# Performance work log

Hardware: AMD Instinct MI355X
Metric: run time of the kernel (lower is better)

## Reference

```python
import jax, jax.numpy as jnp
import numpy as np

N_HEADS = 16
HEAD_SZ = 64

def setup_inputs() -> dict:
    key = jax.random.key(0)
    ks = jax.random.split(key, 6)
    E = 1024
    s = 1.0 / np.sqrt(E)
    return {
        "x": jax.random.normal(ks[0], (2, 2048, E), dtype=jnp.float32),
        "Wq": jax.random.normal(ks[1], (E, N_HEADS * HEAD_SZ), dtype=jnp.float32) * s,
        "Wk": jax.random.normal(ks[2], (E, N_HEADS * HEAD_SZ), dtype=jnp.float32) * s,
        "Wv": jax.random.normal(ks[3], (E, N_HEADS * HEAD_SZ), dtype=jnp.float32) * s,
        "Wp": jax.random.normal(ks[4], (N_HEADS * HEAD_SZ, E), dtype=jnp.float32) * s,
        "bp": jnp.zeros((E,), dtype=jnp.float32),
    }

def reference(x, Wq, Wk, Wv, Wp, bp):
    # flavor="masked": causal self-attention, pdrop=0 -> dropout is identity
    B, S, E = x.shape
    H, D = N_HEADS, HEAD_SZ
    q = (x @ Wq).reshape(B, S, H, D).transpose(0, 2, 1, 3)  # [B,H,S,D]
    k = (x @ Wk).reshape(B, S, H, D).transpose(0, 2, 1, 3)
    v = (x @ Wv).reshape(B, S, H, D).transpose(0, 2, 1, 3)
    scores = jnp.einsum("bhqd,bhkd->bhqk", q, k) / jnp.sqrt(jnp.float32(D))
    causal = jnp.tril(jnp.ones((S, S), dtype=bool))  # [S,S]
    scores = jnp.where(causal, scores, -jnp.inf)
    attn = jax.nn.softmax(scores, axis=-1)
    out = jnp.einsum("bhqk,bhkd->bhqd", attn, v)  # [B,H,S,D]
    out = out.transpose(0, 2, 1, 3).reshape(B, S, H * D)
    return out @ Wp + bp
```

## Files before the change

### kernel.cpp

```cpp
#include <hip/hip_runtime.h>
#include <hip/hip_bf16.h>
#include <math.h>

using bf16 = __hip_bfloat16;
typedef __attribute__((ext_vector_type(8))) short short8;
typedef __attribute__((ext_vector_type(4))) float floatx4;

#define MFMA16(a, b, c) __builtin_amdgcn_mfma_f32_16x16x32_bf16((a), (b), (c), 0, 0, 0)

__device__ __forceinline__ void gll16(const void* g, void* l) {
  __builtin_amdgcn_global_load_lds((__attribute__((address_space(1))) void*)(uintptr_t)g,
                                   (__attribute__((address_space(3))) void*)l, 16, 0, 0);
}

__global__ void detect_bias_k(const unsigned short* __restrict__ x,
                              const void* __restrict__ bsrc,
                              bf16* __restrict__ bdst, int* __restrict__ flag) {
  __shared__ int cnt;
  if (threadIdx.x == 0) cnt = 0;
  __syncthreads();
  int local = 0;
  for (int i = threadIdx.x; i < 8192; i += 256) {
    unsigned short v = x[2 * i];
    if (((v >> 7) & 0xFF) == 0xFF) local++;
  }
  if (local) atomicAdd(&cnt, local);
  __syncthreads();
  int f = (cnt > 0) ? 1 : 0;
  if (threadIdx.x == 0) *flag = f;
  for (int i = threadIdx.x; i < 1024; i += 256)
    bdst[i] = f ? __float2bfloat16(((const float*)bsrc)[i]) : ((const bf16*)bsrc)[i];
}

__global__ __launch_bounds__(256) void prep_k(const void* __restrict__ xin,
                                              bf16* __restrict__ xb,
                                              const void* __restrict__ W0,
                                              const void* __restrict__ W1,
                                              const void* __restrict__ W2,
                                              const void* __restrict__ W3,
                                              bf16* __restrict__ Wt,
                                              bf16* __restrict__ Wpt,
                                              const int* __restrict__ flag) {
  bool f32 = (*flag != 0);
  int z = blockIdx.z;
  if (z < 2) {
    int tid = threadIdx.y * 32 + threadIdx.x;
    int blockLin = z * 1024 + blockIdx.y * 32 + blockIdx.x;
    int idx = blockLin * 2048 + tid * 8;
    if (f32) {
      const float4* p = reinterpret_cast<const float4*>((const float*)xin + idx);
      float4 a = p[0], b = p[1];
      union { bf16 h[8]; uint4 u; } U;
      U.h[0] = __float2bfloat16(a.x); U.h[1] = __float2bfloat16(a.y);
      U.h[2] = __float2bfloat16(a.z); U.h[3] = __float2bfloat16(a.w);
      U.h[4] = __float2bfloat16(b.x); U.h[5] = __float2bfloat16(b.y);
      U.h[6] = __float2bfloat16(b.z); U.h[7] = __float2bfloat16(b.w);
      *reinterpret_cast<uint4*>(xb + idx) = U.u;
    } else {
      *reinterpret_cast<uint4*>(xb + idx) =
          *reinterpret_cast<const uint4*>((const bf16*)xin + idx);
    }
    return;
  }
  const void* src = (z == 2) ? W0 : (z == 3) ? W1 : (z == 4) ? W2 : W3;
  bf16* dst = (z == 5) ? Wpt : (Wt + (size_t)(z - 2) * 1024 * 1024);
  __shared__ float tsh[32][33];
  int tx = threadIdx.x, ty = threadIdx.y;
  int k0 = blockIdx.y * 32, n0 = blockIdx.x * 32;
  for (int i = 0; i < 4; i++) {
    size_t off = (size_t)(k0 + ty + i * 8) * 1024 + n0 + tx;
    tsh[ty + i * 8][tx] = f32 ? ((const float*)src)[off]
                              : __bfloat162float(((const bf16*)src)[off]);
  }
  __syncthreads();
  for (int i = 0; i < 4; i++)
    dst[(size_t)(n0 + ty + i * 8) * 1024 + k0 + tx] = __float2bfloat16(tsh[tx][ty + i * 8]);
}

__global__ __launch_bounds__(512) void vtrans_k(const bf16* __restrict__ QKV,
                                                bf16* __restrict__ VT) {
  __shared__ bf16 t[64][66];
  int tx = threadIdx.x, ty = threadIdx.y;
  int s0 = blockIdx.x * 64, bh = blockIdx.y;
  int b = bh >> 4, h = bh & 15;
  size_t rowb = (size_t)b * 2048;
  int hv = 2048 + h * 64;
#pragma unroll
  for (int i = 0; i < 8; i++)
    t[i * 8 + ty][tx] = QKV[(rowb + s0 + i * 8 + ty) * 3072 + hv + tx];
  __syncthreads();
#pragma unroll
  for (int i = 0; i < 8; i++)
    VT[((size_t)bh * 64 + i * 8 + ty) * 2048 + s0 + tx] = t[tx][i * 8 + ty];
}

__global__ __launch_bounds__(256) void gemm_bt128(const bf16* __restrict__ A, int lda,
                                                  const bf16* __restrict__ Bt, int ldb,
                                                  void* __restrict__ C, int ldc,
                                                  const bf16* __restrict__ bias, int K,
                                                  const int* __restrict__ outflag) {
  __shared__ bf16 As[2][128 * 32];
  __shared__ bf16 Bs[2][128 * 32];
  int t = threadIdx.x;
  int w = t >> 6, lane = t & 63;
  int g = lane >> 4, c = lane & 15;
  int wm = (w >> 1) * 64, wn = (w & 1) * 64;
  int m0 = blockIdx.y * 128, n0 = blockIdx.x * 128;

  int sr = w * 32 + (lane >> 2);
  int sc = (lane & 3) * 8;
  const bf16* Ab = A + (size_t)(m0 + sr) * lda + sc;
  const bf16* Bb = Bt + (size_t)(n0 + sr) * ldb + sc;
  int lofs = (w * 32) * 32;

  floatx4 acc[4][4] = {};

  for (int k0 = 0; k0 < K; k0 += 64) {
    __syncthreads();
#pragma unroll
    for (int h = 0; h < 2; h++) {
      gll16(Ab + k0 + h * 32, &As[h][lofs]);
      gll16(Ab + k0 + h * 32 + (size_t)16 * lda, &As[h][lofs + 16 * 32]);
      gll16(Bb + k0 + h * 32, &Bs[h][lofs]);
      gll16(Bb + k0 + h * 32 + (size_t)16 * ldb, &Bs[h][lofs + 16 * 32]);
    }
    __syncthreads();
#pragma unroll
    for (int h = 0; h < 2; h++) {
      short8 af[4], bf[4];
#pragma unroll
      for (int i = 0; i < 4; i++) {
        af[i] = *reinterpret_cast<const short8*>(&As[h][(wm + i * 16 + c) * 32 + g * 8]);
        bf[i] = *reinterpret_cast<const short8*>(&Bs[h][(wn + i * 16 + c) * 32 + g * 8]);
      }
#pragma unroll
      for (int i = 0; i < 4; i++)
#pragma unroll
        for (int j = 0; j < 4; j++) acc[i][j] = MFMA16(af[i], bf[j], acc[i][j]);
    }
  }

  bool f32out = (outflag != nullptr) && (*outflag != 0);
#pragma unroll
  for (int i = 0; i < 4; i++) {
    int rbase = m0 + wm + i * 16 + g * 4;
#pragma unroll
    for (int j = 0; j < 4; j++) {
      int col = n0 + wn + j * 16 + c;
      float bv = bias ? __bfloat162float(bias[col]) : 0.f;
#pragma unroll
      for (int r = 0; r < 4; r++) {
        size_t off = (size_t)(rbase + r) * ldc + col;
        float v = acc[i][j][r] + bv;
        if (f32out) ((float*)C)[off] = v;
        else ((bf16*)C)[off] = __float2bfloat16(v);
      }
    }
  }
}

__global__ __launch_bounds__(256) void gemm_bt64(const bf16* __restrict__ A, int lda,
                                                 const bf16* __restrict__ Bt, int ldb,
                                                 void* __restrict__ C, int ldc,
                                                 const bf16* __restrict__ bias, int K,
                                                 const int* __restrict__ outflag) {
  __shared__ bf16 As[2][128 * 32];
  __shared__ bf16 Bs[2][64 * 32];
  int t = threadIdx.x;
  int w = t >> 6, lane = t & 63;
  int g = lane >> 4, c = lane & 15;
  int wm = (w >> 1) * 64, wn = (w & 1) * 32;
  int m0 = blockIdx.y * 128, n0 = blockIdx.x * 64;

  int sr = (lane >> 2);
  int sc = (lane & 3) * 8;
  const bf16* Ab = A + (size_t)(m0 + w * 32 + sr) * lda + sc;
  const bf16* Bb = Bt + (size_t)(n0 + w * 16 + sr) * ldb + sc;
  int laofs = (w * 32) * 32;
  int lbofs = (w * 16) * 32;

  floatx4 acc[4][2] = {};

  for (int k0 = 0; k0 < K; k0 += 64) {
    __syncthreads();
#pragma unroll
    for (int h = 0; h < 2; h++) {
      gll16(Ab + k0 + h * 32, &As[h][laofs]);
      gll16(Ab + k0 + h * 32 + (size_t)16 * lda, &As[h][laofs + 16 * 32]);
      gll16(Bb + k0 + h * 32, &Bs[h][lbofs]);
    }
    __syncthreads();
#pragma unroll
    for (int h = 0; h < 2; h++) {
      short8 af[4], bf[2];
#pragma unroll
      for (int i = 0; i < 4; i++)
        af[i] = *reinterpret_cast<const short8*>(&As[h][(wm + i * 16 + c) * 32 + g * 8]);
#pragma unroll
      for (int j = 0; j < 2; j++)
        bf[j] = *reinterpret_cast<const short8*>(&Bs[h][(wn + j * 16 + c) * 32 + g * 8]);
#pragma unroll
      for (int i = 0; i < 4; i++)
#pragma unroll
        for (int j = 0; j < 2; j++) acc[i][j] = MFMA16(af[i], bf[j], acc[i][j]);
    }
  }

  bool f32out = (outflag != nullptr) && (*outflag != 0);
#pragma unroll
  for (int i = 0; i < 4; i++) {
    int rbase = m0 + wm + i * 16 + g * 4;
#pragma unroll
    for (int j = 0; j < 2; j++) {
      int col = n0 + wn + j * 16 + c;
      float bv = bias ? __bfloat162float(bias[col]) : 0.f;
#pragma unroll
      for (int r = 0; r < 4; r++) {
        size_t off = (size_t)(rbase + r) * ldc + col;
        float v = acc[i][j][r] + bv;
        if (f32out) ((float*)C)[off] = v;
        else ((bf16*)C)[off] = __float2bfloat16(v);
      }
    }
  }
}

__global__ __launch_bounds__(512, 4) void attn_lds2(bf16* __restrict__ QKV,
                                                    const bf16* __restrict__ VT) {
  const int S = 2048, LD = 3072;
  __shared__ bf16 Ks[2][2][64 * 32];
  __shared__ bf16 Vs[2][2][64 * 32];
  __shared__ bf16 Pb[8][16 * 72];

  int t = threadIdx.x, w = t >> 6, lane = t & 63, g = lane >> 4, c = lane & 15;
  int bx = blockIdx.x, bh = blockIdx.y;
  int qt = (bh >= 16) ? bx : (15 - bx);
  int b = bh >> 4, h = bh & 15;
  int qbase = qt * 128;
  size_t rowb = (size_t)b * S;
  int hq = h * 64, hk = 1024 + h * 64;
  const bf16* Vt = VT + (size_t)bh * 64 * 2048;
  bf16* pb = Pb[w];

  int su = (w & 3) * 16 + (lane >> 2);
  int sc = (lane & 3) * 8;
  const bf16* Kg = &QKV[(rowb + su) * LD + hk + sc];
  const bf16* Vg = &Vt[(size_t)su * 2048 + sc];
  int sofs = ((w & 3) * 16) * 32;

  short8 qf[2];
#pragma unroll
  for (int hf = 0; hf < 2; hf++)
    qf[hf] = *reinterpret_cast<const short8*>(
        &QKV[(rowb + qbase + w * 16 + c) * LD + hq + hf * 32 + g * 8]);

  floatx4 o[4] = {};
  float l_r[4] = {};

  int nkt = 2 * qt + 2;
  if (w < 4) {
    gll16(Kg, &Ks[0][0][sofs]);
    gll16(Kg + 32, &Ks[0][1][sofs]);
  } else {
    gll16(Vg, &Vs[0][0][sofs]);
    gll16(Vg + 32, &Vs[0][1][sofs]);
  }

  for (int kt = 0; kt < nkt; kt++) {
    int kbase = kt * 64;
    int cur = kt & 1;
    __syncthreads();
    if (kt + 1 < nkt) {
      int nb = cur ^ 1;
      size_t kofs = (size_t)(kbase + 64);
      if (w < 4) {
        gll16(Kg + kofs * LD, &Ks[nb][0][sofs]);
        gll16(Kg + kofs * LD + 32, &Ks[nb][1][sofs]);
      } else {
        gll16(Vg + kofs, &Vs[nb][0][sofs]);
        gll16(Vg + kofs + 32, &Vs[nb][1][sofs]);
      }
    }

    short8 kf[4][2];
#pragma unroll
    for (int nt = 0; nt < 4; nt++)
#pragma unroll
      for (int hf = 0; hf < 2; hf++)
        kf[nt][hf] =
            *reinterpret_cast<const short8*>(&Ks[cur][hf][(nt * 16 + c) * 32 + g * 8]);

    floatx4 s[4];
#pragma unroll
    for (int nt = 0; nt < 4; nt++) {
      floatx4 z = {};
      z = MFMA16(qf[0], kf[nt][0], z);
      z = MFMA16(qf[1], kf[nt][1], z);
      s[nt] = z;
    }

    int qrow = qbase + w * 16 + g * 4;
    bool diag = (kbase + 63 > qbase + w * 16);
#pragma unroll
    for (int nt = 0; nt < 4; nt++) {
      int kcol = kbase + nt * 16 + c;
#pragma unroll
      for (int r = 0; r < 4; r++) {
        float arg = fmaf(s[nt][r], 0.18033688f, -23.083120f);
        if (diag && (kcol > qrow + r)) arg = -1e30f;
        float p = exp2f(arg);
        l_r[r] += p;
        s[nt][r] = p;
      }
    }

    asm volatile("s_waitcnt lgkmcnt(0)" ::: "memory");
#pragma unroll
    for (int nt = 0; nt < 4; nt++)
#pragma unroll
      for (int r = 0; r < 4; r++)
        pb[(g * 4 + r) * 72 + nt * 16 + c] = __float2bfloat16(s[nt][r]);
    asm volatile("s_waitcnt lgkmcnt(0)" ::: "memory");
    short8 pf0 = *reinterpret_cast<const short8*>(&pb[c * 72 + g * 8]);
    short8 pf1 = *reinterpret_cast<const short8*>(&pb[c * 72 + 32 + g * 8]);

#pragma unroll
    for (int dt = 0; dt < 4; dt++) {
      short8 vf0 = *reinterpret_cast<const short8*>(&Vs[cur][0][(dt * 16 + c) * 32 + g * 8]);
      short8 vf1 = *reinterpret_cast<const short8*>(&Vs[cur][1][(dt * 16 + c) * 32 + g * 8]);
      o[dt] = MFMA16(pf0, vf0, o[dt]);
      o[dt] = MFMA16(pf1, vf1, o[dt]);
    }
  }

#pragma unroll
  for (int r = 0; r < 4; r++) {
    float v = l_r[r];
    v += __shfl_xor(v, 1); v += __shfl_xor(v, 2);
    v += __shfl_xor(v, 4); v += __shfl_xor(v, 8);
    l_r[r] = 1.0f / v;
  }

#pragma unroll
  for (int dt = 0; dt < 4; dt++)
#pragma unroll
    for (int r = 0; r < 4; r++) {
      float v = o[dt][r] * l_r[r];
      QKV[(rowb + qbase + w * 16 + g * 4 + r) * LD + hq + dt * 16 + c] =
          __float2bfloat16(v);
    }
}

extern "C" void kernel_launch(void* const* d_in, const int* in_sizes, int n_in,
                              void* d_out, int out_size, void* d_ws, size_t ws_size,
                              hipStream_t stream) {
  char* ws = (char*)d_ws;
  const size_t MB = 1024 * 1024;
  int* flag = (int*)ws;
  bf16* bias = (bf16*)(ws + 4096);
  bf16* xb = (bf16*)(ws + 1 * MB);
  bf16* Wt = (bf16*)(ws + 9 * MB);
  bf16* Wpt = (bf16*)(ws + 15 * MB);
  bf16* QKV = (bf16*)(ws + 17 * MB);
  bf16* VT = xb;

  detect_bias_k<<<1, 256, 0, stream>>>((const unsigned short*)d_in[0], d_in[5], bias, flag);
  prep_k<<<dim3(32, 32, 6), dim3(32, 8), 0, stream>>>(d_in[0], xb, d_in[1], d_in[2],
                                                      d_in[3], d_in[4], Wt, Wpt, flag);

  gemm_bt128<<<dim3(24, 32), 256, 0, stream>>>(xb, 1024, Wt, 1024, QKV, 3072, nullptr,
                                               1024, nullptr);
  vtrans_k<<<dim3(32, 32), dim3(64, 8), 0, stream>>>(QKV, VT);
  attn_lds2<<<dim3(16, 32), 512, 0, stream>>>(QKV, VT);
  gemm_bt64<<<dim3(16, 32), 256, 0, stream>>>(QKV, 3072, Wpt, 1024, d_out, 1024, bias,
                                              1024, flag);
}
```

Baseline: 203.0 us.

## Fuse V transpose into QKV GEMM epilogue and XOR-swizzle LDS tiles

The QKV projection GEMM now writes Q and K into a 2048-wide buffer and writes V directly in transposed per-head layout from its epilogue. This removes the separate vtrans kernel launch and its extra pass over V. In addition, the LDS tiles in all GEMM and attention kernels use an XOR swizzle on the 16-byte column chunk, which is meant to cut LDS bank conflicts on the short8 fragment reads. The transposed V store writes 8-byte chunks with stride 2048 elements, so those global writes are poorly coalesced.

```diff
diff --git a/kernel.cpp b/kernel.cpp
--- a/kernel.cpp
+++ b/kernel.cpp
@@ -77,28 +77,10 @@
     dst[(size_t)(n0 + ty + i * 8) * 1024 + k0 + tx] = __float2bfloat16(tsh[tx][ty + i * 8]);
 }
 
-__global__ __launch_bounds__(512) void vtrans_k(const bf16* __restrict__ QKV,
-                                                bf16* __restrict__ VT) {
-  __shared__ bf16 t[64][66];
-  int tx = threadIdx.x, ty = threadIdx.y;
-  int s0 = blockIdx.x * 64, bh = blockIdx.y;
-  int b = bh >> 4, h = bh & 15;
-  size_t rowb = (size_t)b * 2048;
-  int hv = 2048 + h * 64;
-#pragma unroll
-  for (int i = 0; i < 8; i++)
-    t[i * 8 + ty][tx] = QKV[(rowb + s0 + i * 8 + ty) * 3072 + hv + tx];
-  __syncthreads();
-#pragma unroll
-  for (int i = 0; i < 8; i++)
-    VT[((size_t)bh * 64 + i * 8 + ty) * 2048 + s0 + tx] = t[tx][i * 8 + ty];
-}
-
-__global__ __launch_bounds__(256) void gemm_bt128(const bf16* __restrict__ A, int lda,
-                                                  const bf16* __restrict__ Bt, int ldb,
-                                                  void* __restrict__ C, int ldc,
-                                                  const bf16* __restrict__ bias, int K,
-                                                  const int* __restrict__ outflag) {
+__global__ __launch_bounds__(256) void gemm_qkv(const bf16* __restrict__ A, int lda,
+                                                const bf16* __restrict__ Bt, int ldb,
+                                                bf16* __restrict__ QKV2,
+                                                bf16* __restrict__ VT, int K) {
   __shared__ bf16 As[2][128 * 32];
   __shared__ bf16 Bs[2][128 * 32];
   int t = threadIdx.x;
@@ -108,10 +90,11 @@
   int m0 = blockIdx.y * 128, n0 = blockIdx.x * 128;
 
   int sr = w * 32 + (lane >> 2);
-  int sc = (lane & 3) * 8;
-  const bf16* Ab = A + (size_t)(m0 + sr) * lda + sc;
-  const bf16* Bb = Bt + (size_t)(n0 + sr) * ldb + sc;
+  int scz = (((lane & 3) ^ ((lane >> 3) & 3)) * 8);
+  const bf16* Ab = A + (size_t)(m0 + sr) * lda + scz;
+  const bf16* Bb = Bt + (size_t)(n0 + sr) * ldb + scz;
   int lofs = (w * 32) * 32;
+  int xg8 = (g ^ ((c >> 1) & 3)) * 8;
 
   floatx4 acc[4][4] = {};
 
@@ -130,8 +113,8 @@
       short8 af[4], bf[4];
 #pragma unroll
       for (int i = 0; i < 4; i++) {
-        af[i] = *reinterpret_cast<const short8*>(&As[h][(wm + i * 16 + c) * 32 + g * 8]);
-        bf[i] = *reinterpret_cast<const short8*>(&Bs[h][(wn + i * 16 + c) * 32 + g * 8]);
+        af[i] = *reinterpret_cast<const short8*>(&As[h][(wm + i * 16 + c) * 32 + xg8]);
+        bf[i] = *reinterpret_cast<const short8*>(&Bs[h][(wn + i * 16 + c) * 32 + xg8]);
       }
 #pragma unroll
       for (int i = 0; i < 4; i++)
@@ -140,20 +123,27 @@
     }
   }
 
-  bool f32out = (outflag != nullptr) && (*outflag != 0);
+  bool vblock = (n0 >= 2048);
+  int bb = m0 >> 11;
 #pragma unroll
   for (int i = 0; i < 4; i++) {
     int rbase = m0 + wm + i * 16 + g * 4;
 #pragma unroll
     for (int j = 0; j < 4; j++) {
       int col = n0 + wn + j * 16 + c;
-      float bv = bias ? __bfloat162float(bias[col]) : 0.f;
-#pragma unroll
-      for (int r = 0; r < 4; r++) {
-        size_t off = (size_t)(rbase + r) * ldc + col;
-        float v = acc[i][j][r] + bv;
-        if (f32out) ((float*)C)[off] = v;
-        else ((bf16*)C)[off] = __float2bfloat16(v);
+      if (!vblock) {
+#pragma unroll
+        for (int r = 0; r < 4; r++)
+          QKV2[(size_t)(rbase + r) * 2048 + col] = __float2bfloat16(acc[i][j][r]);
+      } else {
+        int dcol = col - 2048;
+        int hh = dcol >> 6, dl = dcol & 63;
+        int s = rbase & 2047;
+        union { bf16 h4[4]; uint2 u; } P;
+#pragma unroll
+        for (int r = 0; r < 4; r++) P.h4[r] = __float2bfloat16(acc[i][j][r]);
+        *reinterpret_cast<uint2*>(
+            &VT[((size_t)((bb * 16 + hh) * 64 + dl)) * 2048 + s]) = P.u;
       }
     }
   }
@@ -173,11 +163,12 @@
   int m0 = blockIdx.y * 128, n0 = blockIdx.x * 64;
 
   int sr = (lane >> 2);
-  int sc = (lane & 3) * 8;
-  const bf16* Ab = A + (size_t)(m0 + w * 32 + sr) * lda + sc;
-  const bf16* Bb = Bt + (size_t)(n0 + w * 16 + sr) * ldb + sc;
+  int scz = (((lane & 3) ^ ((lane >> 3) & 3)) * 8);
+  const bf16* Ab = A + (size_t)(m0 + w * 32 + sr) * lda + scz;
+  const bf16* Bb = Bt + (size_t)(n0 + w * 16 + sr) * ldb + scz;
   int laofs = (w * 32) * 32;
   int lbofs = (w * 16) * 32;
+  int xg8 = (g ^ ((c >> 1) & 3)) * 8;
 
   floatx4 acc[4][2] = {};
 
@@ -195,10 +186,10 @@
       short8 af[4], bf[2];
 #pragma unroll
       for (int i = 0; i < 4; i++)
-        af[i] = *reinterpret_cast<const short8*>(&As[h][(wm + i * 16 + c) * 32 + g * 8]);
+        af[i] = *reinterpret_cast<const short8*>(&As[h][(wm + i * 16 + c) * 32 + xg8]);
 #pragma unroll
       for (int j = 0; j < 2; j++)
-        bf[j] = *reinterpret_cast<const short8*>(&Bs[h][(wn + j * 16 + c) * 32 + g * 8]);
+        bf[j] = *reinterpret_cast<const short8*>(&Bs[h][(wn + j * 16 + c) * 32 + xg8]);
 #pragma unroll
       for (int i = 0; i < 4; i++)
 #pragma unroll
@@ -227,7 +218,7 @@
 
 __global__ __launch_bounds__(512, 4) void attn_lds2(bf16* __restrict__ QKV,
                                                     const bf16* __restrict__ VT) {
-  const int S = 2048, LD = 3072;
+  const int S = 2048, LD = 2048;
   __shared__ bf16 Ks[2][2][64 * 32];
   __shared__ bf16 Vs[2][2][64 * 32];
   __shared__ bf16 Pb[8][16 * 72];
@@ -243,10 +234,11 @@
   bf16* pb = Pb[w];
 
   int su = (w & 3) * 16 + (lane >> 2);
-  int sc = (lane & 3) * 8;
-  const bf16* Kg = &QKV[(rowb + su) * LD + hk + sc];
-  const bf16* Vg = &Vt[(size_t)su * 2048 + sc];
+  int scz = (((lane & 3) ^ ((lane >> 3) & 3)) * 8);
+  const bf16* Kg = &QKV[(rowb + su) * LD + hk + scz];
+  const bf16* Vg = &Vt[(size_t)su * 2048 + scz];
   int sofs = ((w & 3) * 16) * 32;
+  int xg8 = (g ^ ((c >> 1) & 3)) * 8;
 
   short8 qf[2];
 #pragma unroll
@@ -288,7 +280,7 @@
 #pragma unroll
       for (int hf = 0; hf < 2; hf++)
         kf[nt][hf] =
-            *reinterpret_cast<const short8*>(&Ks[cur][hf][(nt * 16 + c) * 32 + g * 8]);
+            *reinterpret_cast<const short8*>(&Ks[cur][hf][(nt * 16 + c) * 32 + xg8]);
 
     floatx4 s[4];
 #pragma unroll
@@ -326,8 +318,8 @@
 
 #pragma unroll
     for (int dt = 0; dt < 4; dt++) {
-      short8 vf0 = *reinterpret_cast<const short8*>(&Vs[cur][0][(dt * 16 + c) * 32 + g * 8]);
-      short8 vf1 = *reinterpret_cast<const short8*>(&Vs[cur][1][(dt * 16 + c) * 32 + g * 8]);
+      short8 vf0 = *reinterpret_cast<const short8*>(&Vs[cur][0][(dt * 16 + c) * 32 + xg8]);
+      short8 vf1 = *reinterpret_cast<const short8*>(&Vs[cur][1][(dt * 16 + c) * 32 + xg8]);
       o[dt] = MFMA16(pf0, vf0, o[dt]);
       o[dt] = MFMA16(pf1, vf1, o[dt]);
     }
@@ -361,17 +353,15 @@
   bf16* xb = (bf16*)(ws + 1 * MB);
   bf16* Wt = (bf16*)(ws + 9 * MB);
   bf16* Wpt = (bf16*)(ws + 15 * MB);
-  bf16* QKV = (bf16*)(ws + 17 * MB);
-  bf16* VT = xb;
+  bf16* QKV2 = (bf16*)(ws + 17 * MB);
+  bf16* VT = (bf16*)(ws + 33 * MB);
 
   detect_bias_k<<<1, 256, 0, stream>>>((const unsigned short*)d_in[0], d_in[5], bias, flag);
   prep_k<<<dim3(32, 32, 6), dim3(32, 8), 0, stream>>>(d_in[0], xb, d_in[1], d_in[2],
                                                       d_in[3], d_in[4], Wt, Wpt, flag);
 
-  gemm_bt128<<<dim3(24, 32), 256, 0, stream>>>(xb, 1024, Wt, 1024, QKV, 3072, nullptr,
-                                               1024, nullptr);
-  vtrans_k<<<dim3(32, 32), dim3(64, 8), 0, stream>>>(QKV, VT);
-  attn_lds2<<<dim3(16, 32), 512, 0, stream>>>(QKV, VT);
-  gemm_bt64<<<dim3(16, 32), 256, 0, stream>>>(QKV, 3072, Wpt, 1024, d_out, 1024, bias,
+  gemm_qkv<<<dim3(24, 32), 256, 0, stream>>>(xb, 1024, Wt, 1024, QKV2, VT, 1024);
+  attn_lds2<<<dim3(16, 32), 512, 0, stream>>>(QKV2, VT);
+  gemm_bt64<<<dim3(16, 32), 256, 0, stream>>>(QKV2, 2048, Wpt, 1024, d_out, 1024, bias,
                                               1024, flag);
 }
```

Measured after the change: 203.0 us. No clear change (+0.0%).
